# Kernel optimization log

Measured on AMD Instinct MI355X. Metric: run time of the kernel, lower is better.

The kernel has to match this reference:

```python
import jax, jax.numpy as jnp
import numpy as np

INPUT_SIZE = 8
HIDDEN = 64
NUM_CLASSES = 24


def _gru_dir(x_t, Wih, Whh, bih, bhh, reverse):
    """One direction of a GRU layer. x_t: [T, B, in]. Returns [T, B, H] (PyTorch order)."""
    B = x_t.shape[1]
    H = Whh.shape[1]
    h0 = jnp.zeros((B, H), x_t.dtype)
    # Precompute input projections for all timesteps: [T, B, 3H]
    gi_all = jnp.einsum('tbi,gi->tbg', x_t, Wih) + bih

    def step(h, gi):
        gh = h @ Whh.T + bhh
        i_r, i_z, i_n = jnp.split(gi, 3, axis=-1)
        h_r, h_z, h_n = jnp.split(gh, 3, axis=-1)
        r = jax.nn.sigmoid(i_r + h_r)
        z = jax.nn.sigmoid(i_z + h_z)
        n = jnp.tanh(i_n + r * h_n)
        h_new = (1.0 - z) * n + z * h
        return h_new, h_new

    _, out = jax.lax.scan(step, h0, gi_all, reverse=reverse)
    return out  # with reverse=True, out[t] matches PyTorch backward-direction output at t


def _bigru_layer(x, Wf, Uf, bf, cf, Wb, Ub, bb, cb):
    """x: [B, T, in] -> [B, T, 2H]."""
    x_t = jnp.swapaxes(x, 0, 1)  # [T, B, in]
    of = _gru_dir(x_t, Wf, Uf, bf, cf, reverse=False)
    ob = _gru_dir(x_t, Wb, Ub, bb, cb, reverse=True)
    return jnp.swapaxes(jnp.concatenate([of, ob], axis=-1), 0, 1)


def setup_inputs() -> dict:
    key = jax.random.key(0)
    keys = jax.random.split(key, 24)
    B, T = 256, 2048
    k = 1.0 / np.sqrt(HIDDEN)

    def u(kk, shape):
        return jax.random.uniform(kk, shape, jnp.float32, -k, k)

    inp = {"x": jax.random.normal(keys[0], (B, T, INPUT_SIZE), jnp.float32)}
    # GRU layer 0 (input 8), layer 1 (input 2H=128); fwd and bwd directions
    i = 1
    for l, in_dim in [(0, INPUT_SIZE), (1, 2 * HIDDEN)]:
        for d in ['f', 'b']:
            inp[f"Wih_l{l}_{d}"] = u(keys[i], (3 * HIDDEN, in_dim)); i += 1
            inp[f"Whh_l{l}_{d}"] = u(keys[i], (3 * HIDDEN, HIDDEN)); i += 1
            inp[f"bih_l{l}_{d}"] = u(keys[i], (3 * HIDDEN,)); i += 1
            inp[f"bhh_l{l}_{d}"] = u(keys[i], (3 * HIDDEN,)); i += 1
    # Classifier: Linear(128 -> 128), ReLU, Linear(128 -> 24). Dropout = identity (eval).
    inp["W1"] = u(keys[i], (128, 2 * HIDDEN)); i += 1
    inp["b1"] = u(keys[i], (128,)); i += 1
    inp["W2"] = u(keys[i], (NUM_CLASSES, 128)); i += 1
    inp["b2"] = u(keys[i], (NUM_CLASSES,))
    return inp


def reference(x,
              Wih_l0_f, Whh_l0_f, bih_l0_f, bhh_l0_f,
              Wih_l0_b, Whh_l0_b, bih_l0_b, bhh_l0_b,
              Wih_l1_f, Whh_l1_f, bih_l1_f, bhh_l1_f,
              Wih_l1_b, Whh_l1_b, bih_l1_b, bhh_l1_b,
              W1, b1, W2, b2):
    h0 = _bigru_layer(x, Wih_l0_f, Whh_l0_f, bih_l0_f, bhh_l0_f,
                      Wih_l0_b, Whh_l0_b, bih_l0_b, bhh_l0_b)
    # inter-layer dropout is inactive at inference (eval mode)
    h1 = _bigru_layer(h0, Wih_l1_f, Whh_l1_f, bih_l1_f, bhh_l1_f,
                      Wih_l1_b, Whh_l1_b, bih_l1_b, bhh_l1_b)
    last = h1[:, -1, :]  # [B, 2H]
    hid = jax.nn.relu(last @ W1.T + b1)
    logits = hid @ W2.T + b2
    return logits
```

## Files before the change

### kernel.cpp

```cpp
#include <hip/hip_runtime.h>
#include <cstdint>
#include <cstddef>

#define T_LEN 2048
#define B_SZ  256
#define H_SZ  64

typedef float v2f __attribute__((ext_vector_type(2)));
typedef unsigned short ushort_t;

__device__ __forceinline__ v2f v2fma(v2f a, v2f b, v2f c) {
#if __has_builtin(__builtin_elementwise_fma)
    return __builtin_elementwise_fma(a, b, c);
#else
    v2f r; r.x = fmaf(a.x, b.x, c.x); r.y = fmaf(a.y, b.y, c.y); return r;
#endif
}

__device__ __forceinline__ float sigmf(float x) {
    return 1.0f / (1.0f + __expf(-x));
}
__device__ __forceinline__ float tanhf_fast(float x) {
    return 1.0f - 2.0f / (__expf(2.0f * x) + 1.0f);
}

__device__ __forceinline__ ushort_t f2bf(float f) {
    unsigned int u = __float_as_uint(f);
    u += 0x7fffu + ((u >> 16) & 1u);
    return (ushort_t)(u >> 16);
}
__device__ __forceinline__ float bf_lo(unsigned int u) {
    return __uint_as_float(u << 16);
}
__device__ __forceinline__ float bf_hi(unsigned int u) {
    return __uint_as_float(u & 0xffff0000u);
}

__global__ void __launch_bounds__(64, 1)
l0_kernel(const float* __restrict__ x,
          const float* __restrict__ Wih_f, const float* __restrict__ Whh_f,
          const float* __restrict__ bih_f, const float* __restrict__ bhh_f,
          const float* __restrict__ Wih_b, const float* __restrict__ Whh_b,
          const float* __restrict__ bih_b, const float* __restrict__ bhh_b,
          ushort_t* __restrict__ l0bf, float* __restrict__ l0T)
{
    const int bid = blockIdx.x;
    const int dir = bid & 1;
    const int b   = bid >> 1;
    const int j   = threadIdx.x;

    const float* __restrict__ Wih = dir ? Wih_b : Wih_f;
    const float* __restrict__ Whh = dir ? Whh_b : Whh_f;
    const float* __restrict__ bih = dir ? bih_b : bih_f;
    const float* __restrict__ bhh = dir ? bhh_b : bhh_f;

    v2f wr[32], wz[32], wn[32];
    {
        const v2f* p0 = (const v2f*)(Whh + (size_t)j * H_SZ);
        const v2f* p1 = (const v2f*)(Whh + (size_t)(j + 64) * H_SZ);
        const v2f* p2 = (const v2f*)(Whh + (size_t)(j + 128) * H_SZ);
        #pragma unroll
        for (int k = 0; k < 32; ++k) { wr[k] = p0[k]; wz[k] = p1[k]; wn[k] = p2[k]; }
    }
    float ur[8], uz[8], un[8];
    #pragma unroll
    for (int i = 0; i < 8; ++i) {
        ur[i] = Wih[(size_t)j * 8 + i];
        uz[i] = Wih[(size_t)(j + 64) * 8 + i];
        un[i] = Wih[(size_t)(j + 128) * 8 + i];
    }
    const float b_rz_r = bih[j] + bhh[j];
    const float b_rz_z = bih[j + 64] + bhh[j + 64];
    const float b_in   = bih[j + 128];
    const float b_hn   = bhh[j + 128];

    __shared__ __align__(16) float hs[H_SZ];
    float h = 0.0f;
    hs[j] = 0.0f;
    __syncthreads();

    const float* __restrict__ xb = x + (size_t)b * T_LEN * 8;
    ushort_t* __restrict__ outp = l0bf + (size_t)b * 128 + dir * 64 + j;

    #pragma unroll 1
    for (int s = 0; s < T_LEN; ++s) {
        const int tt = dir ? (T_LEN - 1 - s) : s;
        const float4* xp = (const float4*)(xb + (size_t)tt * 8);
        const float4 x0 = xp[0];
        const float4 x1 = xp[1];

        float gr = b_rz_r, gz = b_rz_z, gn = b_in;
        gr = fmaf(ur[0], x0.x, gr); gr = fmaf(ur[1], x0.y, gr);
        gr = fmaf(ur[2], x0.z, gr); gr = fmaf(ur[3], x0.w, gr);
        gr = fmaf(ur[4], x1.x, gr); gr = fmaf(ur[5], x1.y, gr);
        gr = fmaf(ur[6], x1.z, gr); gr = fmaf(ur[7], x1.w, gr);
        gz = fmaf(uz[0], x0.x, gz); gz = fmaf(uz[1], x0.y, gz);
        gz = fmaf(uz[2], x0.z, gz); gz = fmaf(uz[3], x0.w, gz);
        gz = fmaf(uz[4], x1.x, gz); gz = fmaf(uz[5], x1.y, gz);
        gz = fmaf(uz[6], x1.z, gz); gz = fmaf(uz[7], x1.w, gz);
        gn = fmaf(un[0], x0.x, gn); gn = fmaf(un[1], x0.y, gn);
        gn = fmaf(un[2], x0.z, gn); gn = fmaf(un[3], x0.w, gn);
        gn = fmaf(un[4], x1.x, gn); gn = fmaf(un[5], x1.y, gn);
        gn = fmaf(un[6], x1.z, gn); gn = fmaf(un[7], x1.w, gn);

        v2f ar0 = {0.f,0.f}, ar1 = {0.f,0.f};
        v2f az0 = {0.f,0.f}, az1 = {0.f,0.f};
        v2f an0 = {0.f,0.f}, an1 = {0.f,0.f};
        const float4* hs4 = (const float4*)hs;
        #pragma unroll
        for (int k4 = 0; k4 < 16; ++k4) {
            const float4 hv = hs4[k4];
            const v2f h0 = {hv.x, hv.y};
            const v2f h1 = {hv.z, hv.w};
            ar0 = v2fma(wr[2*k4],   h0, ar0);
            ar1 = v2fma(wr[2*k4+1], h1, ar1);
            az0 = v2fma(wz[2*k4],   h0, az0);
            az1 = v2fma(wz[2*k4+1], h1, az1);
            an0 = v2fma(wn[2*k4],   h0, an0);
            an1 = v2fma(wn[2*k4+1], h1, an1);
        }
        const float hr = (ar0.x + ar0.y) + (ar1.x + ar1.y);
        const float hz = (az0.x + az0.y) + (az1.x + az1.y);
        const float hn = (an0.x + an0.y) + (an1.x + an1.y) + b_hn;

        const float r = sigmf(gr + hr);
        const float z = sigmf(gz + hz);
        const float n = tanhf_fast(gn + r * hn);
        h = fmaf(z, h - n, n);

        hs[j] = h;
        outp[(size_t)tt * (B_SZ * 128)] = f2bf(h);
        if (tt == T_LEN - 1)
            l0T[(size_t)b * 128 + dir * 64 + j] = h;
        __syncthreads();
    }
}

__global__ void __launch_bounds__(192, 1)
l1_kernel(const ushort_t* __restrict__ l0bf,
          const float* __restrict__ Wih, const float* __restrict__ Whh,
          const float* __restrict__ bih, const float* __restrict__ bhh,
          float* __restrict__ hf)
{
    const int b  = blockIdx.x;
    const int wv = threadIdx.x >> 6;
    const int j  = threadIdx.x & 63;

    __shared__ __align__(16) float hs[H_SZ];
    __shared__ __align__(16) float gip[2][2][192];

    v2f wA[32], wB[32], wC[32];
    if (wv == 0) {
        const v2f* p0 = (const v2f*)(Whh + (size_t)j * H_SZ);
        const v2f* p1 = (const v2f*)(Whh + (size_t)(j + 64) * H_SZ);
        const v2f* p2 = (const v2f*)(Whh + (size_t)(j + 128) * H_SZ);
        #pragma unroll
        for (int k = 0; k < 32; ++k) { wA[k] = p0[k]; wB[k] = p1[k]; wC[k] = p2[k]; }
        hs[j] = 0.0f;
    } else {
        const int kb = (wv - 1) * 64;
        const v2f* p0 = (const v2f*)(Wih + (size_t)j * 128 + kb);
        const v2f* p1 = (const v2f*)(Wih + (size_t)(j + 64) * 128 + kb);
        const v2f* p2 = (const v2f*)(Wih + (size_t)(j + 128) * 128 + kb);
        #pragma unroll
        for (int k = 0; k < 32; ++k) { wA[k] = p0[k]; wB[k] = p1[k]; wC[k] = p2[k]; }
    }
    const float b_rz_r = bih[j] + bhh[j];
    const float b_rz_z = bih[j + 64] + bhh[j + 64];
    const float b_in   = bih[j + 128];
    const float b_hn   = bhh[j + 128];

    float h = 0.0f;

    auto produce = [&](int tp) {
        const int bf = tp & 1;
        const uint4* ap = (const uint4*)(l0bf + ((size_t)tp * B_SZ + b) * 128 + (wv - 1) * 64);
        v2f aA0 = {0.f,0.f}, aA1 = {0.f,0.f};
        v2f aB0 = {0.f,0.f}, aB1 = {0.f,0.f};
        v2f aC0 = {0.f,0.f}, aC1 = {0.f,0.f};
        #pragma unroll
        for (int q = 0; q < 8; ++q) {
            const uint4 u4 = ap[q];
            const v2f a0 = {bf_lo(u4.x), bf_hi(u4.x)};
            const v2f a1 = {bf_lo(u4.y), bf_hi(u4.y)};
            const v2f a2 = {bf_lo(u4.z), bf_hi(u4.z)};
            const v2f a3 = {bf_lo(u4.w), bf_hi(u4.w)};
            aA0 = v2fma(wA[4*q],   a0, aA0);
            aA1 = v2fma(wA[4*q+1], a1, aA1);
            aA0 = v2fma(wA[4*q+2], a2, aA0);
            aA1 = v2fma(wA[4*q+3], a3, aA1);
            aB0 = v2fma(wB[4*q],   a0, aB0);
            aB1 = v2fma(wB[4*q+1], a1, aB1);
            aB0 = v2fma(wB[4*q+2], a2, aB0);
            aB1 = v2fma(wB[4*q+3], a3, aB1);
            aC0 = v2fma(wC[4*q],   a0, aC0);
            aC1 = v2fma(wC[4*q+1], a1, aC1);
            aC0 = v2fma(wC[4*q+2], a2, aC0);
            aC1 = v2fma(wC[4*q+3], a3, aC1);
        }
        gip[bf][wv - 1][j]       = (aA0.x + aA0.y) + (aA1.x + aA1.y);
        gip[bf][wv - 1][j + 64]  = (aB0.x + aB0.y) + (aB1.x + aB1.y);
        gip[bf][wv - 1][j + 128] = (aC0.x + aC0.y) + (aC1.x + aC1.y);
    };

    if (wv > 0) produce(0);
    __syncthreads();

    #pragma unroll 1
    for (int t = 0; t < T_LEN; ++t) {
        if (wv == 0) {
            const int bf = t & 1;
            float gr = gip[bf][0][j]       + gip[bf][1][j]       + b_rz_r;
            float gz = gip[bf][0][j + 64]  + gip[bf][1][j + 64]  + b_rz_z;
            float gn = gip[bf][0][j + 128] + gip[bf][1][j + 128] + b_in;

            v2f ar0 = {0.f,0.f}, ar1 = {0.f,0.f};
            v2f az0 = {0.f,0.f}, az1 = {0.f,0.f};
            v2f an0 = {0.f,0.f}, an1 = {0.f,0.f};
            const float4* hs4 = (const float4*)hs;
            #pragma unroll
            for (int k4 = 0; k4 < 16; ++k4) {
                const float4 hv = hs4[k4];
                const v2f h0 = {hv.x, hv.y};
                const v2f h1 = {hv.z, hv.w};
                ar0 = v2fma(wA[2*k4],   h0, ar0);
                ar1 = v2fma(wA[2*k4+1], h1, ar1);
                az0 = v2fma(wB[2*k4],   h0, az0);
                az1 = v2fma(wB[2*k4+1], h1, az1);
                an0 = v2fma(wC[2*k4],   h0, an0);
                an1 = v2fma(wC[2*k4+1], h1, an1);
            }
            const float hr = (ar0.x + ar0.y) + (ar1.x + ar1.y);
            const float hz = (az0.x + az0.y) + (az1.x + az1.y);
            const float hn = (an0.x + an0.y) + (an1.x + an1.y) + b_hn;

            const float r = sigmf(gr + hr);
            const float z = sigmf(gz + hz);
            const float n = tanhf_fast(gn + r * hn);
            h = fmaf(z, h - n, n);
            hs[j] = h;
        } else if (t + 1 < T_LEN) {
            produce(t + 1);
        }
        __syncthreads();
    }

    if (wv == 0) hf[(size_t)b * 64 + j] = h;
}

__global__ void __launch_bounds__(192)
head_kernel(const float* __restrict__ l0T,
            const float* __restrict__ Wih_b1, const float* __restrict__ bih_b1,
            const float* __restrict__ bhh_b1,
            const float* __restrict__ hf,
            const float* __restrict__ W1, const float* __restrict__ b1,
            const float* __restrict__ W2, const float* __restrict__ b2,
            float* __restrict__ out)
{
    const int b   = blockIdx.x;
    const int tid = threadIdx.x;

    __shared__ __align__(16) float a_s[128];
    __shared__ __align__(16) float gi_s[192];
    __shared__ __align__(16) float last_s[128];
    __shared__ __align__(16) float hid_s[128];

    if (tid < 128)
        a_s[tid] = l0T[(size_t)b * 128 + tid];
    __syncthreads();

    {
        float acc = bih_b1[tid];
        const float4* wrow = (const float4*)(Wih_b1 + (size_t)tid * 128);
        const float4* av4  = (const float4*)a_s;
        #pragma unroll
        for (int k4 = 0; k4 < 32; ++k4) {
            const float4 w  = wrow[k4];
            const float4 av = av4[k4];
            acc = fmaf(w.x, av.x, acc); acc = fmaf(w.y, av.y, acc);
            acc = fmaf(w.z, av.z, acc); acc = fmaf(w.w, av.w, acc);
        }
        gi_s[tid] = acc;
    }
    __syncthreads();

    if (tid < 64) {
        const float r = sigmf(gi_s[tid]      + bhh_b1[tid]);
        const float z = sigmf(gi_s[tid + 64] + bhh_b1[tid + 64]);
        const float n = tanhf_fast(gi_s[tid + 128] + r * bhh_b1[tid + 128]);
        last_s[64 + tid] = (1.0f - z) * n;
        last_s[tid]      = hf[(size_t)b * 64 + tid];
    }
    __syncthreads();

    if (tid < 128) {
        float acc = b1[tid];
        const float4* wrow = (const float4*)(W1 + (size_t)tid * 128);
        const float4* lv4  = (const float4*)last_s;
        #pragma unroll
        for (int k4 = 0; k4 < 32; ++k4) {
            const float4 w = wrow[k4];
            const float4 l = lv4[k4];
            acc = fmaf(w.x, l.x, acc); acc = fmaf(w.y, l.y, acc);
            acc = fmaf(w.z, l.z, acc); acc = fmaf(w.w, l.w, acc);
        }
        hid_s[tid] = fmaxf(acc, 0.0f);
    }
    __syncthreads();

    if (tid < 24) {
        float acc = b2[tid];
        const float4* wrow = (const float4*)(W2 + (size_t)tid * 128);
        const float4* hv4  = (const float4*)hid_s;
        #pragma unroll
        for (int k4 = 0; k4 < 32; ++k4) {
            const float4 w = wrow[k4];
            const float4 hv = hv4[k4];
            acc = fmaf(w.x, hv.x, acc); acc = fmaf(w.y, hv.y, acc);
            acc = fmaf(w.z, hv.z, acc); acc = fmaf(w.w, hv.w, acc);
        }
        out[(size_t)b * 24 + tid] = acc;
    }
}

extern "C" void kernel_launch(void* const* d_in, const int* in_sizes, int n_in,
                              void* d_out, int out_size, void* d_ws, size_t ws_size,
                              hipStream_t stream)
{
    const float* x        = (const float*)d_in[0];
    const float* Wih_l0_f = (const float*)d_in[1];
    const float* Whh_l0_f = (const float*)d_in[2];
    const float* bih_l0_f = (const float*)d_in[3];
    const float* bhh_l0_f = (const float*)d_in[4];
    const float* Wih_l0_b = (const float*)d_in[5];
    const float* Whh_l0_b = (const float*)d_in[6];
    const float* bih_l0_b = (const float*)d_in[7];
    const float* bhh_l0_b = (const float*)d_in[8];
    const float* Wih_l1_f = (const float*)d_in[9];
    const float* Whh_l1_f = (const float*)d_in[10];
    const float* bih_l1_f = (const float*)d_in[11];
    const float* bhh_l1_f = (const float*)d_in[12];
    const float* Wih_l1_b = (const float*)d_in[13];
    const float* bih_l1_b = (const float*)d_in[15];
    const float* bhh_l1_b = (const float*)d_in[16];
    const float* W1 = (const float*)d_in[17];
    const float* b1 = (const float*)d_in[18];
    const float* W2 = (const float*)d_in[19];
    const float* b2 = (const float*)d_in[20];

    ushort_t* l0bf = (ushort_t*)d_ws;
    float*    l0T  = (float*)((char*)d_ws + (size_t)T_LEN * B_SZ * 128 * sizeof(ushort_t));
    float*    hf   = l0T + (size_t)B_SZ * 128;

    hipLaunchKernelGGL(l0_kernel, dim3(2 * B_SZ), dim3(64), 0, stream,
                       x, Wih_l0_f, Whh_l0_f, bih_l0_f, bhh_l0_f,
                       Wih_l0_b, Whh_l0_b, bih_l0_b, bhh_l0_b, l0bf, l0T);

    hipLaunchKernelGGL(l1_kernel, dim3(B_SZ), dim3(192), 0, stream,
                       l0bf, Wih_l1_f, Whh_l1_f, bih_l1_f, bhh_l1_f, hf);

    hipLaunchKernelGGL(head_kernel, dim3(B_SZ), dim3(192), 0, stream,
                       l0T, Wih_l1_b, bih_l1_b, bhh_l1_b, hf,
                       W1, b1, W2, b2, (float*)d_out);
}
```

Before: 2.731 ms.

## Prefetch inputs and replace full barriers with LDS-only barriers in GRU kernels

```diff
diff --git a/kernel.cpp b/kernel.cpp
--- a/kernel.cpp
+++ b/kernel.cpp
@@ -34,6 +34,11 @@
 }
 __device__ __forceinline__ float bf_hi(unsigned int u) {
     return __uint_as_float(u & 0xffff0000u);
+}
+
+__device__ __forceinline__ void barrier_lds_only() {
+    asm volatile("s_waitcnt lgkmcnt(0)" ::: "memory");
+    __builtin_amdgcn_s_barrier();
 }
 
 __global__ void __launch_bounds__(64, 1)
@@ -77,31 +82,38 @@
     __shared__ __align__(16) float hs[H_SZ];
     float h = 0.0f;
     hs[j] = 0.0f;
-    __syncthreads();
 
     const float* __restrict__ xb = x + (size_t)b * T_LEN * 8;
     ushort_t* __restrict__ outp = l0bf + (size_t)b * 128 + dir * 64 + j;
 
+    int tt = dir ? (T_LEN - 1) : 0;
+    const int tstep = dir ? -1 : 1;
+    float4 cx0, cx1;
+    {
+        const float4* xp = (const float4*)(xb + (size_t)tt * 8);
+        cx0 = xp[0]; cx1 = xp[1];
+    }
+
     #pragma unroll 1
     for (int s = 0; s < T_LEN; ++s) {
-        const int tt = dir ? (T_LEN - 1 - s) : s;
-        const float4* xp = (const float4*)(xb + (size_t)tt * 8);
-        const float4 x0 = xp[0];
-        const float4 x1 = xp[1];
+        const int ntt = (s + 1 < T_LEN) ? (tt + tstep) : tt;
+        const float4* xq = (const float4*)(xb + (size_t)ntt * 8);
+        const float4 nx0 = xq[0];
+        const float4 nx1 = xq[1];
 
         float gr = b_rz_r, gz = b_rz_z, gn = b_in;
-        gr = fmaf(ur[0], x0.x, gr); gr = fmaf(ur[1], x0.y, gr);
-        gr = fmaf(ur[2], x0.z, gr); gr = fmaf(ur[3], x0.w, gr);
-        gr = fmaf(ur[4], x1.x, gr); gr = fmaf(ur[5], x1.y, gr);
-        gr = fmaf(ur[6], x1.z, gr); gr = fmaf(ur[7], x1.w, gr);
-        gz = fmaf(uz[0], x0.x, gz); gz = fmaf(uz[1], x0.y, gz);
-        gz = fmaf(uz[2], x0.z, gz); gz = fmaf(uz[3], x0.w, gz);
-        gz = fmaf(uz[4], x1.x, gz); gz = fmaf(uz[5], x1.y, gz);
-        gz = fmaf(uz[6], x1.z, gz); gz = fmaf(uz[7], x1.w, gz);
-        gn = fmaf(un[0], x0.x, gn); gn = fmaf(un[1], x0.y, gn);
-        gn = fmaf(un[2], x0.z, gn); gn = fmaf(un[3], x0.w, gn);
-        gn = fmaf(un[4], x1.x, gn); gn = fmaf(un[5], x1.y, gn);
-        gn = fmaf(un[6], x1.z, gn); gn = fmaf(un[7], x1.w, gn);
+        gr = fmaf(ur[0], cx0.x, gr); gr = fmaf(ur[1], cx0.y, gr);
+        gr = fmaf(ur[2], cx0.z, gr); gr = fmaf(ur[3], cx0.w, gr);
+        gr = fmaf(ur[4], cx1.x, gr); gr = fmaf(ur[5], cx1.y, gr);
+        gr = fmaf(ur[6], cx1.z, gr); gr = fmaf(ur[7], cx1.w, gr);
+        gz = fmaf(uz[0], cx0.x, gz); gz = fmaf(uz[1], cx0.y, gz);
+        gz = fmaf(uz[2], cx0.z, gz); gz = fmaf(uz[3], cx0.w, gz);
+        gz = fmaf(uz[4], cx1.x, gz); gz = fmaf(uz[5], cx1.y, gz);
+        gz = fmaf(uz[6], cx1.z, gz); gz = fmaf(uz[7], cx1.w, gz);
+        gn = fmaf(un[0], cx0.x, gn); gn = fmaf(un[1], cx0.y, gn);
+        gn = fmaf(un[2], cx0.z, gn); gn = fmaf(un[3], cx0.w, gn);
+        gn = fmaf(un[4], cx1.x, gn); gn = fmaf(un[5], cx1.y, gn);
+        gn = fmaf(un[6], cx1.z, gn); gn = fmaf(un[7], cx1.w, gn);
 
         v2f ar0 = {0.f,0.f}, ar1 = {0.f,0.f};
         v2f az0 = {0.f,0.f}, az1 = {0.f,0.f};
@@ -132,9 +144,77 @@
         outp[(size_t)tt * (B_SZ * 128)] = f2bf(h);
         if (tt == T_LEN - 1)
             l0T[(size_t)b * 128 + dir * 64 + j] = h;
-        __syncthreads();
-    }
-}
+
+        cx0 = nx0; cx1 = nx1;
+        tt = ntt;
+    }
+}
+
+#define L1_LOADROW(DST, TP) do {                                              \
+    const uint4* _ap = (const uint4*)(l0bf +                                  \
+        ((size_t)(TP) * B_SZ + b) * 128 + (wv - 1) * 64);                     \
+    _Pragma("unroll")                                                         \
+    for (int _q = 0; _q < 8; ++_q) DST[_q] = _ap[_q];                         \
+} while (0)
+
+#define L1_COMPUTE_GI(BF, SRC) do {                                           \
+    v2f aA0 = {0.f,0.f}, aA1 = {0.f,0.f};                                     \
+    v2f aB0 = {0.f,0.f}, aB1 = {0.f,0.f};                                     \
+    v2f aC0 = {0.f,0.f}, aC1 = {0.f,0.f};                                     \
+    _Pragma("unroll")                                                         \
+    for (int _q = 0; _q < 8; ++_q) {                                          \
+        const uint4 u4 = SRC[_q];                                             \
+        const v2f a0 = {bf_lo(u4.x), bf_hi(u4.x)};                            \
+        const v2f a1 = {bf_lo(u4.y), bf_hi(u4.y)};                            \
+        const v2f a2 = {bf_lo(u4.z), bf_hi(u4.z)};                            \
+        const v2f a3 = {bf_lo(u4.w), bf_hi(u4.w)};                            \
+        aA0 = v2fma(wA[4*_q],   a0, aA0);                                     \
+        aA1 = v2fma(wA[4*_q+1], a1, aA1);                                     \
+        aA0 = v2fma(wA[4*_q+2], a2, aA0);                                     \
+        aA1 = v2fma(wA[4*_q+3], a3, aA1);                                     \
+        aB0 = v2fma(wB[4*_q],   a0, aB0);                                     \
+        aB1 = v2fma(wB[4*_q+1], a1, aB1);                                     \
+        aB0 = v2fma(wB[4*_q+2], a2, aB0);                                     \
+        aB1 = v2fma(wB[4*_q+3], a3, aB1);                                     \
+        aC0 = v2fma(wC[4*_q],   a0, aC0);                                     \
+        aC1 = v2fma(wC[4*_q+1], a1, aC1);                                     \
+        aC0 = v2fma(wC[4*_q+2], a2, aC0);                                     \
+        aC1 = v2fma(wC[4*_q+3], a3, aC1);                                     \
+    }                                                                         \
+    gip[BF][wv - 1][j]       = (aA0.x + aA0.y) + (aA1.x + aA1.y);             \
+    gip[BF][wv - 1][j + 64]  = (aB0.x + aB0.y) + (aB1.x + aB1.y);             \
+    gip[BF][wv - 1][j + 128] = (aC0.x + aC0.y) + (aC1.x + aC1.y);             \
+} while (0)
+
+#define L1_CONSUMER_STEP(BF) do {                                             \
+    float gr = gip[BF][0][j]       + gip[BF][1][j]       + b_rz_r;            \
+    float gz = gip[BF][0][j + 64]  + gip[BF][1][j + 64]  + b_rz_z;            \
+    float gn = gip[BF][0][j + 128] + gip[BF][1][j + 128] + b_in;              \
+    v2f ar0 = {0.f,0.f}, ar1 = {0.f,0.f};                                     \
+    v2f az0 = {0.f,0.f}, az1 = {0.f,0.f};                                     \
+    v2f an0 = {0.f,0.f}, an1 = {0.f,0.f};                                     \
+    const float4* hs4 = (const float4*)hs;                                    \
+    _Pragma("unroll")                                                         \
+    for (int _k = 0; _k < 16; ++_k) {                                         \
+        const float4 hv = hs4[_k];                                            \
+        const v2f h0 = {hv.x, hv.y};                                          \
+        const v2f h1 = {hv.z, hv.w};                                          \
+        ar0 = v2fma(wA[2*_k],   h0, ar0);                                     \
+        ar1 = v2fma(wA[2*_k+1], h1, ar1);                                     \
+        az0 = v2fma(wB[2*_k],   h0, az0);                                     \
+        az1 = v2fma(wB[2*_k+1], h1, az1);                                     \
+        an0 = v2fma(wC[2*_k],   h0, an0);                                     \
+        an1 = v2fma(wC[2*_k+1], h1, an1);                                     \
+    }                                                                         \
+    const float hr = (ar0.x + ar0.y) + (ar1.x + ar1.y);                       \
+    const float hz = (az0.x + az0.y) + (az1.x + az1.y);                       \
+    const float hn = (an0.x + an0.y) + (an1.x + an1.y) + b_hn;                \
+    const float r = sigmf(gr + hr);                                           \
+    const float z = sigmf(gz + hz);                                           \
+    const float n = tanhf_fast(gn + r * hn);                                  \
+    h = fmaf(z, h - n, n);                                                    \
+    hs[j] = h;                                                                \
+} while (0)
 
 __global__ void __launch_bounds__(192, 1)
 l1_kernel(const ushort_t* __restrict__ l0bf,
@@ -171,78 +251,36 @@
     const float b_hn   = bhh[j + 128];
 
     float h = 0.0f;
-
-    auto produce = [&](int tp) {
-        const int bf = tp & 1;
-        const uint4* ap = (const uint4*)(l0bf + ((size_t)tp * B_SZ + b) * 128 + (wv - 1) * 64);
-        v2f aA0 = {0.f,0.f}, aA1 = {0.f,0.f};
-        v2f aB0 = {0.f,0.f}, aB1 = {0.f,0.f};
-        v2f aC0 = {0.f,0.f}, aC1 = {0.f,0.f};
-        #pragma unroll
-        for (int q = 0; q < 8; ++q) {
-            const uint4 u4 = ap[q];
-            const v2f a0 = {bf_lo(u4.x), bf_hi(u4.x)};
-            const v2f a1 = {bf_lo(u4.y), bf_hi(u4.y)};
-            const v2f a2 = {bf_lo(u4.z), bf_hi(u4.z)};
-            const v2f a3 = {bf_lo(u4.w), bf_hi(u4.w)};
-            aA0 = v2fma(wA[4*q],   a0, aA0);
-            aA1 = v2fma(wA[4*q+1], a1, aA1);
-            aA0 = v2fma(wA[4*q+2], a2, aA0);
-            aA1 = v2fma(wA[4*q+3], a3, aA1);
-            aB0 = v2fma(wB[4*q],   a0, aB0);
-            aB1 = v2fma(wB[4*q+1], a1, aB1);
-            aB0 = v2fma(wB[4*q+2], a2, aB0);
-            aB1 = v2fma(wB[4*q+3], a3, aB1);
-            aC0 = v2fma(wC[4*q],   a0, aC0);
-            aC1 = v2fma(wC[4*q+1], a1, aC1);
-            aC0 = v2fma(wC[4*q+2], a2, aC0);
-            aC1 = v2fma(wC[4*q+3], a3, aC1);
-        }
-        gip[bf][wv - 1][j]       = (aA0.x + aA0.y) + (aA1.x + aA1.y);
-        gip[bf][wv - 1][j + 64]  = (aB0.x + aB0.y) + (aB1.x + aB1.y);
-        gip[bf][wv - 1][j + 128] = (aC0.x + aC0.y) + (aC1.x + aC1.y);
-    };
-
-    if (wv > 0) produce(0);
-    __syncthreads();
+    uint4 rbE[8], rbO[8];
+
+    if (wv > 0) {
+        uint4 r0[8];
+        L1_LOADROW(r0, 0);
+        L1_COMPUTE_GI(0, r0);
+        L1_LOADROW(rbO, 1);
+        L1_LOADROW(rbE, 2);
+    }
+    barrier_lds_only();
 
     #pragma unroll 1
-    for (int t = 0; t < T_LEN; ++t) {
+    for (int t = 0; t < T_LEN; t += 2) {
         if (wv == 0) {
-            const int bf = t & 1;
-            float gr = gip[bf][0][j]       + gip[bf][1][j]       + b_rz_r;
-            float gz = gip[bf][0][j + 64]  + gip[bf][1][j + 64]  + b_rz_z;
-            float gn = gip[bf][0][j + 128] + gip[bf][1][j + 128] + b_in;
-
-            v2f ar0 = {0.f,0.f}, ar1 = {0.f,0.f};
-            v2f az0 = {0.f,0.f}, az1 = {0.f,0.f};
-            v2f an0 = {0.f,0.f}, an1 = {0.f,0.f};
-            const float4* hs4 = (const float4*)hs;
-            #pragma unroll
-            for (int k4 = 0; k4 < 16; ++k4) {
-                const float4 hv = hs4[k4];
-                const v2f h0 = {hv.x, hv.y};
-                const v2f h1 = {hv.z, hv.w};
-                ar0 = v2fma(wA[2*k4],   h0, ar0);
-                ar1 = v2fma(wA[2*k4+1], h1, ar1);
-                az0 = v2fma(wB[2*k4],   h0, az0);
-                az1 = v2fma(wB[2*k4+1], h1, az1);
-                an0 = v2fma(wC[2*k4],   h0, an0);
-                an1 = v2fma(wC[2*k4+1], h1, an1);
-            }
-            const float hr = (ar0.x + ar0.y) + (ar1.x + ar1.y);
-            const float hz = (az0.x + az0.y) + (az1.x + az1.y);
-            const float hn = (an0.x + an0.y) + (an1.x + an1.y) + b_hn;
-
-            const float r = sigmf(gr + hr);
-            const float z = sigmf(gz + hz);
-            const float n = tanhf_fast(gn + r * hn);
-            h = fmaf(z, h - n, n);
-            hs[j] = h;
-        } else if (t + 1 < T_LEN) {
-            produce(t + 1);
-        }
-        __syncthreads();
+            L1_CONSUMER_STEP(0);
+        } else {
+            L1_COMPUTE_GI(1, rbO);
+            int tp = t + 3; if (tp > T_LEN - 1) tp = T_LEN - 1;
+            L1_LOADROW(rbO, tp);
+        }
+        barrier_lds_only();
+
+        if (wv == 0) {
+            L1_CONSUMER_STEP(1);
+        } else if (t + 2 < T_LEN) {
+            L1_COMPUTE_GI(0, rbE);
+            int tp = t + 4; if (tp > T_LEN - 1) tp = T_LEN - 1;
+            L1_LOADROW(rbE, tp);
+        }
+        barrier_lds_only();
     }
 
     if (wv == 0) hf[(size_t)b * 64 + j] = h;
```

After: 3.034 ms. 11.1% more time.
